# Performance work log

Hardware: AMD Instinct MI355X
Metric: run time of the kernel (lower is better)

Reference implementation:

```python
import jax, jax.numpy as jnp
import numpy as np

N_DRUG, N_MICROBE = 1500, 1572
N = N_DRUG + N_MICROBE          # 3072 nodes
F_IN = 1546                     # raw feature dim (fc1: 1546 -> 256)
D0 = 256                        # GCN input dim after fc1
H1 = H2 = 128                   # GCN hidden dims (H1 + H2 = 256)
B = 16384                       # number of (left,right) query pairs


def _sym_norm(A):
    # D^{-1/2} A D^{-1/2} (no self loops), zeros kept for isolated nodes
    deg = A.sum(axis=1)
    d = jnp.where(deg > 0, jax.lax.rsqrt(deg), 0.0)
    return A * d[:, None] * d[None, :]


def _compute_inf(adj, L):
    # dl.compute_inf: L-hop influence = L-th power of sym-normalized adjacency
    An = _sym_norm(adj)
    M = An
    for _ in range(L - 1):
        M = M @ An
    return M


def _gcn_norm(W):
    # GCNConv normalization: add self loops (weight 1), sym-normalize by weighted degree
    Ahat = W + jnp.eye(W.shape[0], dtype=W.dtype)
    deg = Ahat.sum(axis=1)
    d = jnp.where(deg > 0, jax.lax.rsqrt(deg), 0.0)
    return Ahat * d[:, None] * d[None, :]


def _glorot(key, shape):
    return jax.random.normal(key, shape, dtype=jnp.float32) / np.sqrt(shape[0])


def setup_inputs() -> dict:
    key = jax.random.key(0)
    ks = jax.random.split(key, 24)
    u = jax.random.uniform(ks[0], (N, N), dtype=jnp.float32)
    w = jax.random.uniform(ks[1], (N, N), dtype=jnp.float32)
    adj = jnp.where(u < 0.01, w, 0.0)
    adj = jnp.maximum(adj, adj.T)
    X = jax.random.normal(ks[2], (N, F_IN), dtype=jnp.float32)
    left = jax.random.randint(ks[3], (B,), 0, N)
    right = jax.random.randint(ks[4], (B,), 0, N)
    return dict(
        left=left, right=right, X=X, adj=adj, threshold=jnp.float32(1e-4),
        W_fc1=_glorot(ks[5], (F_IN, D0)), b_fc1=jnp.zeros((D0,), jnp.float32),
        Wg1=_glorot(ks[6], (D0, H1)), bg1=jnp.zeros((H1,), jnp.float32),
        Wg2=_glorot(ks[7], (H1, H2)), bg2=jnp.zeros((H2,), jnp.float32),
        Wg3=_glorot(ks[8], (D0, H1)), bg3=jnp.zeros((H1,), jnp.float32),
        Wg4=_glorot(ks[9], (H1, H2)), bg4=jnp.zeros((H2,), jnp.float32),
        Wg5=_glorot(ks[10], (D0, H1)), bg5=jnp.zeros((H1,), jnp.float32),
        Wg6=_glorot(ks[11], (H1, H2)), bg6=jnp.zeros((H2,), jnp.float32),
        cnn_k=jax.random.normal(ks[12], (1, 3, 3, 3), dtype=jnp.float32) * 0.1,
        cnn_b=jnp.zeros((1,), jnp.float32),
        W_a=_glorot(ks[13], (2 * (H1 + H2), 64)), b_a=jnp.zeros((64,), jnp.float32),
        W_b=_glorot(ks[14], (64, 2)), b_b=jnp.zeros((2,), jnp.float32),
    )


def reference(left, right, X, adj, threshold,
              W_fc1, b_fc1, Wg1, bg1, Wg2, bg2, Wg3, bg3, Wg4, bg4,
              Wg5, bg5, Wg6, bg6, cnn_k, cnn_b, W_a, b_a, W_b, b_b):
    X0 = jax.nn.relu(X @ W_fc1 + b_fc1)  # fc1: [N, 1546] -> [N, 256]

    def branch(mask_src, Wa, ba, Wb, bb):
        # dynamically thresholded edges carry the ORIGINAL adj weights
        Wadj = jnp.where(mask_src > threshold, adj, 0.0)
        An = _gcn_norm(Wadj)                       # [N, N]
        e1 = jax.nn.relu(An @ (X0 @ Wa) + ba)      # GCNConv 1
        e2 = jax.nn.relu(An @ (e1 @ Wb) + bb)      # GCNConv 2
        return jnp.concatenate([e1, e2], axis=1)   # [N, 256]

    emb_l2 = branch(_compute_inf(adj, 2), Wg1, bg1, Wg2, bg2)
    emb_l1 = branch(_compute_inf(adj, 1), Wg3, bg3, Wg4, bg4)
    emb_l0 = branch(adj, Wg5, bg5, Wg6, bg6)

    emb = jnp.stack([emb_l0, emb_l1, emb_l2], axis=0)[None]  # [1, 3, N, 256]
    conv = jax.lax.conv_general_dilated(
        emb, cnn_k, window_strides=(1, 1), padding=[(2, 2), (2, 2)],
        rhs_dilation=(2, 2), dimension_numbers=('NCHW', 'OIHW', 'NCHW'))
    emb_all = conv[0, 0] + cnn_b[0]                # [N, 256]

    pair = jnp.concatenate([emb_all[left], emb_all[right]], axis=1)  # [B, 512]
    h = jax.nn.relu(pair @ W_a + b_a)              # dropout is identity at eval
    logits = h @ W_b + b_b                         # [B, 2]
    return logits, emb_all
```

## Files before the change

### kernel.cpp

```cpp
#include <hip/hip_runtime.h>

#define NN 3072
#define FIN 1546
#define MAXR 192
#define KSPLIT 7
#define KSL 221

__global__ __launch_bounds__(256) void csr_k(const float* __restrict__ adj,
                                             int* __restrict__ cols, float* __restrict__ vals,
                                             int* __restrict__ cnt, float* __restrict__ dvec) {
    int i = blockIdx.x * 4 + (threadIdx.x >> 6);
    int lane = threadIdx.x & 63;
    const float* row = adj + (size_t)i * NN;
    float s = 0.f; int count = 0;
    int base = i * MAXR;
    for (int c = 0; c < NN; c += 64) {
        float a = row[c + lane];
        s += a;
        unsigned long long m = __ballot(a != 0.f);
        if (a != 0.f) {
            int pos = count + __popcll(m & ((1ull << lane) - 1ull));
            if (pos < MAXR) { cols[base + pos] = c + lane; vals[base + pos] = a; }
        }
        count += __popcll(m);
    }
    for (int off = 32; off; off >>= 1) s += __shfl_xor(s, off);
    if (lane == 0) {
        cnt[i] = count < MAXR ? count : MAXR;
        dvec[i] = (s > 0.f) ? 1.0f / sqrtf(s) : 0.f;
    }
}

__global__ __launch_bounds__(256) void fc1s_k(const float* __restrict__ A,
                                              const float* __restrict__ B,
                                              float* __restrict__ Cpart) {
    __shared__ float Ast[16][68];
    __shared__ float Bs[16][64];
    int tid = threadIdx.x;
    int tx = tid & 15, ty = tid >> 4;
    int i0 = blockIdx.x * 64, c0 = blockIdx.y * 64;
    int z = blockIdx.z;
    int ks = z * KSL;
    int ke = (ks + KSL < FIN) ? ks + KSL : FIN;
    int sr = tid >> 4, sk = tid & 15;
    int bk = tid >> 4, bc4 = (tid & 15) << 2;

    float ap[4]; float4 bp;
    #pragma unroll
    for (int u = 0; u < 4; u++)
        ap[u] = (ks + sk < ke) ? A[(size_t)(i0 + sr + u * 16) * FIN + ks + sk] : 0.f;
    bp = (ks + bk < ke) ? *(const float4*)&B[(size_t)(ks + bk) * 256 + c0 + bc4]
                        : make_float4(0.f, 0.f, 0.f, 0.f);

    float acc[4][4];
    #pragma unroll
    for (int r = 0; r < 4; r++)
        #pragma unroll
        for (int c = 0; c < 4; c++) acc[r][c] = 0.f;

    for (int kt = ks; kt < ke; kt += 16) {
        __syncthreads();
        #pragma unroll
        for (int u = 0; u < 4; u++) Ast[sk][sr + u * 16] = ap[u];
        *(float4*)&Bs[bk][bc4] = bp;
        __syncthreads();
        int kn = kt + 16;
        if (kn < ke) {
            #pragma unroll
            for (int u = 0; u < 4; u++)
                ap[u] = (kn + sk < ke) ? A[(size_t)(i0 + sr + u * 16) * FIN + kn + sk] : 0.f;
            bp = (kn + bk < ke) ? *(const float4*)&B[(size_t)(kn + bk) * 256 + c0 + bc4]
                                : make_float4(0.f, 0.f, 0.f, 0.f);
        }
        #pragma unroll
        for (int kk = 0; kk < 16; kk++) {
            float4 a = *(const float4*)&Ast[kk][ty * 4];
            float4 b = *(const float4*)&Bs[kk][tx * 4];
            const float* av = (const float*)&a;
            const float* bv = (const float*)&b;
            #pragma unroll
            for (int r = 0; r < 4; r++)
                #pragma unroll
                for (int c = 0; c < 4; c++) acc[r][c] += av[r] * bv[c];
        }
    }
    float* outp = Cpart + (size_t)z * NN * 256;
    #pragma unroll
    for (int r = 0; r < 4; r++) {
        int row = i0 + ty * 4 + r;
        float4 v = make_float4(acc[r][0], acc[r][1], acc[r][2], acc[r][3]);
        *(float4*)&outp[(size_t)row * 256 + c0 + tx * 4] = v;
    }
}

__global__ void reduce7_k(const float* __restrict__ Cpart, const float* __restrict__ bias,
                          float* __restrict__ X0) {
    int idx4 = blockIdx.x * 256 + threadIdx.x;
    int c4 = (idx4 & 63) << 2;
    float4 s = ((const float4*)Cpart)[idx4];
    #pragma unroll
    for (int z = 1; z < KSPLIT; z++) {
        float4 t = ((const float4*)(Cpart + (size_t)z * NN * 256))[idx4];
        s.x += t.x; s.y += t.y; s.z += t.z; s.w += t.w;
    }
    float4 b = *(const float4*)&bias[c4];
    s.x = fmaxf(s.x + b.x, 0.f); s.y = fmaxf(s.y + b.y, 0.f);
    s.z = fmaxf(s.z + b.z, 0.f); s.w = fmaxf(s.w + b.w, 0.f);
    ((float4*)X0)[idx4] = s;
}

__global__ __launch_bounds__(256) void maskall_k(const int* __restrict__ cols,
                                                 const float* __restrict__ vals,
                                                 const int* __restrict__ cnt,
                                                 const float* __restrict__ dvec,
                                                 const float* __restrict__ thrp,
                                                 int* __restrict__ mcols,
                                                 float* __restrict__ mvals,
                                                 int* __restrict__ mcnt,
                                                 float* __restrict__ db) {
    __shared__ float ds[NN];
    __shared__ int lcols[MAXR];
    __shared__ float lvals[MAXR];
    __shared__ int lcnt;
    __shared__ float osum;
    int i = blockIdx.x, tid = threadIdx.x, mode = blockIdx.y;
    mcols += (size_t)mode * NN * MAXR;
    mvals += (size_t)mode * NN * MAXR;
    mcnt  += (size_t)mode * NN;
    db    += (size_t)mode * NN;
    int ni = cnt[i], base = i * MAXR;
    float thr = *thrp;
    float di = dvec[i];

    if (mode < 2) {
        if (tid == 0) lcnt = 0;
        __syncthreads();
        float s = 0.f;
        if (tid < ni) {
            int j = cols[base + tid];
            float a = vals[base + tid];
            float m = (mode == 0) ? a : a * di * dvec[j];
            if (m > thr) {
                int p = atomicAdd(&lcnt, 1);
                mcols[base + p] = j;
                mvals[base + p] = a;
                s = a;
            }
        }
        ds[tid] = s; __syncthreads();
        for (int off = 128; off; off >>= 1) {
            if (tid < off) ds[tid] += ds[tid + off];
            __syncthreads();
        }
        if (tid == 0) {
            mcnt[i] = lcnt;
            db[i] = 1.0f / sqrtf(ds[0] + 1.0f);
        }
        return;
    }

    if (tid == 0) { osum = 0.f; lcnt = 0; }
    for (int j = tid; j < NN; j += 256) ds[j] = 0.f;
    __syncthreads();
    for (int t = tid; t < ni; t += 256) {
        int j = cols[base + t];
        float a = vals[base + t];
        lcols[t] = j; lvals[t] = a;
        ds[j] = a * dvec[j] * dvec[j];
    }
    __syncthreads();
    int lane = tid & 63, wv = tid >> 6;
    for (int o = wv; o < ni; o += 4) {
        int j = lcols[o];
        int nj = cnt[j], bj = j * MAXR;
        float dot = 0.f;
        for (int t = lane; t < nj; t += 64)
            dot += vals[bj + t] * ds[cols[bj + t]];
        for (int off = 32; off; off >>= 1) dot += __shfl_xor(dot, off);
        if (lane == 0 && di * dvec[j] * dot > thr) {
            int p = atomicAdd(&lcnt, 1);
            mcols[base + p] = j;
            mvals[base + p] = lvals[o];
            atomicAdd(&osum, lvals[o]);
        }
    }
    __syncthreads();
    if (tid == 0) {
        mcnt[i] = lcnt;
        db[i] = 1.0f / sqrtf(osum + 1.0f);
    }
}

__global__ __launch_bounds__(256) void gemm3_k(const float* __restrict__ A, int aplane, int lda,
                                               const float* __restrict__ B0,
                                               const float* __restrict__ B1,
                                               const float* __restrict__ B2,
                                               int K, float* __restrict__ out) {
    __shared__ float Ast[16][68];
    __shared__ float Bs[16][64];
    int tid = threadIdx.x;
    int tx = tid & 15, ty = tid >> 4;
    int i0 = blockIdx.x * 64, c0 = blockIdx.y * 64;
    int z = blockIdx.z;
    const float* Ab = A + (size_t)z * aplane;
    const float* B = (z == 0) ? B0 : (z == 1) ? B1 : B2;
    float* outp = out + (size_t)z * NN * 128;
    int sr = tid >> 4, sk = tid & 15;
    int bk = tid >> 4, bc4 = (tid & 15) << 2;

    float ap[4]; float4 bp;
    #pragma unroll
    for (int u = 0; u < 4; u++) ap[u] = Ab[(size_t)(i0 + sr + u * 16) * lda + sk];
    bp = *(const float4*)&B[(size_t)bk * 128 + c0 + bc4];

    float acc[4][4];
    #pragma unroll
    for (int r = 0; r < 4; r++)
        #pragma unroll
        for (int c = 0; c < 4; c++) acc[r][c] = 0.f;

    for (int kt = 0; kt < K; kt += 16) {
        __syncthreads();
        #pragma unroll
        for (int u = 0; u < 4; u++) Ast[sk][sr + u * 16] = ap[u];
        *(float4*)&Bs[bk][bc4] = bp;
        __syncthreads();
        int kn = kt + 16;
        if (kn < K) {
            #pragma unroll
            for (int u = 0; u < 4; u++) ap[u] = Ab[(size_t)(i0 + sr + u * 16) * lda + kn + sk];
            bp = *(const float4*)&B[(size_t)(kn + bk) * 128 + c0 + bc4];
        }
        #pragma unroll
        for (int kk = 0; kk < 16; kk++) {
            float4 a = *(const float4*)&Ast[kk][ty * 4];
            float4 b = *(const float4*)&Bs[kk][tx * 4];
            const float* av = (const float*)&a;
            const float* bv = (const float*)&b;
            #pragma unroll
            for (int r = 0; r < 4; r++)
                #pragma unroll
                for (int c = 0; c < 4; c++) acc[r][c] += av[r] * bv[c];
        }
    }
    #pragma unroll
    for (int r = 0; r < 4; r++) {
        int row = i0 + ty * 4 + r;
        float4 v = make_float4(acc[r][0], acc[r][1], acc[r][2], acc[r][3]);
        *(float4*)&outp[(size_t)row * 128 + c0 + tx * 4] = v;
    }
}

__global__ __launch_bounds__(256) void spmm3_k(const int* __restrict__ mcols,
                                               const float* __restrict__ mvals,
                                               const int* __restrict__ mcnt,
                                               const float* __restrict__ db,
                                               const float* __restrict__ Xin,
                                               const float* __restrict__ bias0,
                                               const float* __restrict__ bias1,
                                               const float* __restrict__ bias2,
                                               float* __restrict__ outA,
                                               float* __restrict__ embf, int coff) {
    __shared__ float lcoef[MAXR];
    __shared__ int lj[MAXR];
    __shared__ float4 part[8][32];
    int i = blockIdx.x, tid = threadIdx.x, b = blockIdx.y;
    mcols += (size_t)b * NN * MAXR;
    mvals += (size_t)b * NN * MAXR;
    mcnt  += (size_t)b * NN;
    db    += (size_t)b * NN;
    const float* Xb = Xin + (size_t)b * NN * 128;
    const float* bias = (b == 0) ? bias0 : (b == 1) ? bias1 : bias2;
    float dbi = db[i];
    int n = mcnt[i], base = i * MAXR;
    if (tid < n) {
        int j = mcols[base + tid];
        lj[tid] = j;
        lcoef[tid] = mvals[base + tid] * dbi * db[j];
    }
    __syncthreads();
    int g = tid >> 5, c4 = (tid & 31) << 2;
    float4 acc = make_float4(0.f, 0.f, 0.f, 0.f);
    if (g == 0) {
        float4 x = *(const float4*)&Xb[(size_t)i * 128 + c4];
        float d2 = dbi * dbi;
        acc = make_float4(d2 * x.x, d2 * x.y, d2 * x.z, d2 * x.w);
    }
    for (int t = g; t < n; t += 8) {
        float cf = lcoef[t];
        float4 x = *(const float4*)&Xb[(size_t)lj[t] * 128 + c4];
        acc.x += cf * x.x; acc.y += cf * x.y; acc.z += cf * x.z; acc.w += cf * x.w;
    }
    part[g][tid & 31] = acc;
    __syncthreads();
    if (tid < 32) {
        float4 s = part[0][tid];
        #pragma unroll
        for (int gg = 1; gg < 8; gg++) {
            float4 t4 = part[gg][tid];
            s.x += t4.x; s.y += t4.y; s.z += t4.z; s.w += t4.w;
        }
        int cc = tid << 2;
        float4 bv = *(const float4*)&bias[cc];
        s.x = fmaxf(s.x + bv.x, 0.f); s.y = fmaxf(s.y + bv.y, 0.f);
        s.z = fmaxf(s.z + bv.z, 0.f); s.w = fmaxf(s.w + bv.w, 0.f);
        if (outA) *(float4*)&outA[((size_t)b * NN + i) * 128 + cc] = s;
        *(float4*)&embf[((size_t)b * NN + i) * 256 + coff + cc] = s;
    }
}

__global__ __launch_bounds__(256) void conv3f_k(const float* __restrict__ emb,
                                                const float* __restrict__ ck,
                                                const float* __restrict__ cb,
                                                float* __restrict__ outf) {
    __shared__ float rows[3][3][256];
    int n = blockIdx.x, c = threadIdx.x;
    #pragma unroll
    for (int i = 0; i < 3; i++)
        #pragma unroll
        for (int kh = 0; kh < 3; kh++) {
            int nn2 = n + 2 * kh - 2;
            rows[i][kh][c] = (nn2 >= 0 && nn2 < NN) ? emb[((size_t)i * NN + nn2) * 256 + c] : 0.f;
        }
    __syncthreads();
    float s = cb[0];
    #pragma unroll
    for (int i = 0; i < 3; i++)
        #pragma unroll
        for (int kh = 0; kh < 3; kh++)
            #pragma unroll
            for (int kw = 0; kw < 3; kw++) {
                int cc = c + 2 * kw - 2;
                if (cc >= 0 && cc < 256)
                    s += rows[i][kh][cc] * ck[(i * 3 + kh) * 3 + kw];
            }
    outf[(size_t)n * 256 + c] = s;
}

__global__ __launch_bounds__(256) void gemmUV_k(const float* __restrict__ A,
                                                const float* __restrict__ Wa,
                                                float* __restrict__ uvp) {
    __shared__ float Ast[16][68];
    __shared__ float Bs[16][64];
    int tid = threadIdx.x;
    int tx = tid & 15, ty = tid >> 4;
    int i0 = blockIdx.x * 64;
    int half = blockIdx.y;
    int z = blockIdx.z;
    int ks = z * 128;
    const float* Bb = Wa + (half ? 256 * 64 : 0);
    int sr = tid >> 4, sk = tid & 15;
    int bk = tid >> 4, bc4 = (tid & 15) << 2;

    float ap[4]; float4 bp;
    #pragma unroll
    for (int u = 0; u < 4; u++) ap[u] = A[(size_t)(i0 + sr + u * 16) * 256 + ks + sk];
    bp = *(const float4*)&Bb[(size_t)(ks + bk) * 64 + bc4];

    float acc[4][4];
    #pragma unroll
    for (int r = 0; r < 4; r++)
        #pragma unroll
        for (int c = 0; c < 4; c++) acc[r][c] = 0.f;

    for (int kt = ks; kt < ks + 128; kt += 16) {
        __syncthreads();
        #pragma unroll
        for (int u = 0; u < 4; u++) Ast[sk][sr + u * 16] = ap[u];
        *(float4*)&Bs[bk][bc4] = bp;
        __syncthreads();
        int kn = kt + 16;
        if (kn < ks + 128) {
            #pragma unroll
            for (int u = 0; u < 4; u++) ap[u] = A[(size_t)(i0 + sr + u * 16) * 256 + kn + sk];
            bp = *(const float4*)&Bb[(size_t)(kn + bk) * 64 + bc4];
        }
        #pragma unroll
        for (int kk = 0; kk < 16; kk++) {
            float4 a = *(const float4*)&Ast[kk][ty * 4];
            float4 b = *(const float4*)&Bs[kk][tx * 4];
            const float* av = (const float*)&a;
            const float* bv = (const float*)&b;
            #pragma unroll
            for (int r = 0; r < 4; r++)
                #pragma unroll
                for (int c = 0; c < 4; c++) acc[r][c] += av[r] * bv[c];
        }
    }
    float* outp = uvp + (size_t)z * NN * 128;
    #pragma unroll
    for (int r = 0; r < 4; r++) {
        int row = i0 + ty * 4 + r;
        float4 v = make_float4(acc[r][0], acc[r][1], acc[r][2], acc[r][3]);
        *(float4*)&outp[(size_t)row * 128 + half * 64 + tx * 4] = v;
    }
}

__global__ __launch_bounds__(256) void pairuv_k(const int* __restrict__ left,
                                                const int* __restrict__ right,
                                                const float* __restrict__ uvp,
                                                const float* __restrict__ ba,
                                                const float* __restrict__ Wb,
                                                const float* __restrict__ bb,
                                                float* __restrict__ out) {
    int tid = threadIdx.x;
    int w = tid >> 6, c = tid & 63;
    int base = blockIdx.x * 16 + w * 4;
    const float* u0 = uvp;
    const float* u1 = uvp + (size_t)NN * 128;
    float bac = ba[c];
    float w0 = Wb[c * 2], w1 = Wb[c * 2 + 1];
    float b0 = bb[0], b1 = bb[1];
    #pragma unroll
    for (int pp = 0; pp < 4; pp++) {
        int row = base + pp;
        int l = left[row], r = right[row];
        float h = u0[(size_t)l * 128 + c] + u1[(size_t)l * 128 + c]
                + u0[(size_t)r * 128 + 64 + c] + u1[(size_t)r * 128 + 64 + c] + bac;
        h = fmaxf(h, 0.f);
        float s0 = h * w0, s1 = h * w1;
        for (int off = 32; off; off >>= 1) {
            s0 += __shfl_xor(s0, off);
            s1 += __shfl_xor(s1, off);
        }
        if (c == 0) {
            out[row * 2]     = s0 + b0;
            out[row * 2 + 1] = s1 + b1;
        }
    }
}

extern "C" void kernel_launch(void* const* d_in, const int* in_sizes, int n_in,
                              void* d_out, int out_size, void* d_ws, size_t ws_size,
                              hipStream_t stream) {
    const int* left  = (const int*)d_in[0];
    const int* right = (const int*)d_in[1];
    const float* X    = (const float*)d_in[2];
    const float* adj  = (const float*)d_in[3];
    const float* thr  = (const float*)d_in[4];
    const float* Wfc1 = (const float*)d_in[5];
    const float* bfc1 = (const float*)d_in[6];
    const float* Wga[3] = { (const float*)d_in[15], (const float*)d_in[11], (const float*)d_in[7] };
    const float* bga[3] = { (const float*)d_in[16], (const float*)d_in[12], (const float*)d_in[8] };
    const float* Wgb[3] = { (const float*)d_in[17], (const float*)d_in[13], (const float*)d_in[9] };
    const float* bgb[3] = { (const float*)d_in[18], (const float*)d_in[14], (const float*)d_in[10] };
    const float* cnnk = (const float*)d_in[19];
    const float* cnnb = (const float*)d_in[20];
    const float* Wa_  = (const float*)d_in[21];
    const float* ba_  = (const float*)d_in[22];
    const float* Wb_  = (const float*)d_in[23];
    const float* bb_  = (const float*)d_in[24];

    char* p = (char*)d_ws;
    auto take = [&](size_t n) { char* q = p; p += (n + 255) & ~(size_t)255; return q; };
    float* dvec = (float*)take(NN * 4);
    float* db3  = (float*)take((size_t)3 * NN * 4);
    int*   cnt  = (int*)take(NN * 4);
    int*   mcnt3 = (int*)take((size_t)3 * NN * 4);
    int*   cols = (int*)take((size_t)NN * MAXR * 4);
    float* vals = (float*)take((size_t)NN * MAXR * 4);
    int*   mcols3 = (int*)take((size_t)3 * NN * MAXR * 4);
    float* mvals3 = (float*)take((size_t)3 * NN * MAXR * 4);
    float* X0    = (float*)take((size_t)NN * 256 * 4);
    float* XWall = (float*)take((size_t)3 * NN * 128 * 4);
    float* e1all = (float*)take((size_t)3 * NN * 128 * 4);
    float* HW2all= (float*)take((size_t)3 * NN * 128 * 4);
    float* embf  = (float*)take((size_t)3 * NN * 256 * 4);
    float* Cpart = XWall;
    float* uvp = embf;

    float* out_logits = (float*)d_out;
    float* out_emb = out_logits + 32768;

    csr_k<<<NN / 4, 256, 0, stream>>>(adj, cols, vals, cnt, dvec);
    fc1s_k<<<dim3(NN / 64, 4, KSPLIT), 256, 0, stream>>>(X, Wfc1, Cpart);
    reduce7_k<<<NN * 64 / 256, 256, 0, stream>>>(Cpart, bfc1, X0);

    maskall_k<<<dim3(NN, 3), 256, 0, stream>>>(cols, vals, cnt, dvec, thr,
                                               mcols3, mvals3, mcnt3, db3);

    gemm3_k<<<dim3(NN / 64, 2, 3), 256, 0, stream>>>(X0, 0, 256, Wga[0], Wga[1], Wga[2], 256, XWall);
    spmm3_k<<<dim3(NN, 3), 256, 0, stream>>>(mcols3, mvals3, mcnt3, db3, XWall,
                                             bga[0], bga[1], bga[2], e1all, embf, 0);
    gemm3_k<<<dim3(NN / 64, 2, 3), 256, 0, stream>>>(e1all, NN * 128, 128, Wgb[0], Wgb[1], Wgb[2], 128, HW2all);
    spmm3_k<<<dim3(NN, 3), 256, 0, stream>>>(mcols3, mvals3, mcnt3, db3, HW2all,
                                             bgb[0], bgb[1], bgb[2], (float*)0, embf, 128);

    conv3f_k<<<NN, 256, 0, stream>>>(embf, cnnk, cnnb, out_emb);
    gemmUV_k<<<dim3(NN / 64, 2, 2), 256, 0, stream>>>(out_emb, Wa_, uvp);
    pairuv_k<<<16384 / 16, 256, 0, stream>>>(left, right, uvp, ba_, Wb_, bb_, out_logits);
}
```

Baseline: 339.2 us.

## Compute fc1 with bf16x3 split MFMA instead of FP32 SIMT GEMM

```diff
diff --git a/kernel.cpp b/kernel.cpp
--- a/kernel.cpp
+++ b/kernel.cpp
@@ -2,9 +2,13 @@
 
 #define NN 3072
 #define FIN 1546
+#define KP 1568
 #define MAXR 192
 #define KSPLIT 7
-#define KSL 221
+#define KSLICE 224
+
+typedef __attribute__((ext_vector_type(8))) __bf16 bf16x8;
+typedef __attribute__((ext_vector_type(4))) float f32x4;
 
 __global__ __launch_bounds__(256) void csr_k(const float* __restrict__ adj,
                                              int* __restrict__ cols, float* __restrict__ vals,
@@ -31,65 +35,69 @@
     }
 }
 
-__global__ __launch_bounds__(256) void fc1s_k(const float* __restrict__ A,
-                                              const float* __restrict__ B,
+__global__ void xsplit_k(const float* __restrict__ X, __bf16* __restrict__ Xh,
+                         __bf16* __restrict__ Xl) {
+    int idx = blockIdx.x * 256 + threadIdx.x;
+    int i = idx / KP, c = idx - i * KP;
+    float x = (c < FIN) ? X[(size_t)i * FIN + c] : 0.f;
+    __bf16 h = (__bf16)x;
+    Xh[idx] = h;
+    Xl[idx] = (__bf16)(x - (float)h);
+}
+
+__global__ void wsplit_k(const float* __restrict__ W, __bf16* __restrict__ WhT,
+                         __bf16* __restrict__ WlT) {
+    int idx = blockIdx.x * 256 + threadIdx.x;
+    int c = idx / KP, k = idx - c * KP;
+    float x = (k < FIN) ? W[(size_t)k * 256 + c] : 0.f;
+    __bf16 h = (__bf16)x;
+    WhT[idx] = h;
+    WlT[idx] = (__bf16)(x - (float)h);
+}
+
+__global__ __launch_bounds__(256) void fc1m_k(const __bf16* __restrict__ Xh,
+                                              const __bf16* __restrict__ Xl,
+                                              const __bf16* __restrict__ WhT,
+                                              const __bf16* __restrict__ WlT,
                                               float* __restrict__ Cpart) {
-    __shared__ float Ast[16][68];
-    __shared__ float Bs[16][64];
     int tid = threadIdx.x;
-    int tx = tid & 15, ty = tid >> 4;
+    int w = tid >> 6, lane = tid & 63;
+    int m = lane & 15, q = lane >> 4;
     int i0 = blockIdx.x * 64, c0 = blockIdx.y * 64;
     int z = blockIdx.z;
-    int ks = z * KSL;
-    int ke = (ks + KSL < FIN) ? ks + KSL : FIN;
-    int sr = tid >> 4, sk = tid & 15;
-    int bk = tid >> 4, bc4 = (tid & 15) << 2;
-
-    float ap[4]; float4 bp;
-    #pragma unroll
-    for (int u = 0; u < 4; u++)
-        ap[u] = (ks + sk < ke) ? A[(size_t)(i0 + sr + u * 16) * FIN + ks + sk] : 0.f;
-    bp = (ks + bk < ke) ? *(const float4*)&B[(size_t)(ks + bk) * 256 + c0 + bc4]
-                        : make_float4(0.f, 0.f, 0.f, 0.f);
-
-    float acc[4][4];
-    #pragma unroll
-    for (int r = 0; r < 4; r++)
-        #pragma unroll
-        for (int c = 0; c < 4; c++) acc[r][c] = 0.f;
-
-    for (int kt = ks; kt < ke; kt += 16) {
-        __syncthreads();
-        #pragma unroll
-        for (int u = 0; u < 4; u++) Ast[sk][sr + u * 16] = ap[u];
-        *(float4*)&Bs[bk][bc4] = bp;
-        __syncthreads();
-        int kn = kt + 16;
-        if (kn < ke) {
-            #pragma unroll
-            for (int u = 0; u < 4; u++)
-                ap[u] = (kn + sk < ke) ? A[(size_t)(i0 + sr + u * 16) * FIN + kn + sk] : 0.f;
-            bp = (kn + bk < ke) ? *(const float4*)&B[(size_t)(kn + bk) * 256 + c0 + bc4]
-                                : make_float4(0.f, 0.f, 0.f, 0.f);
-        }
-        #pragma unroll
-        for (int kk = 0; kk < 16; kk++) {
-            float4 a = *(const float4*)&Ast[kk][ty * 4];
-            float4 b = *(const float4*)&Bs[kk][tx * 4];
-            const float* av = (const float*)&a;
-            const float* bv = (const float*)&b;
-            #pragma unroll
-            for (int r = 0; r < 4; r++)
-                #pragma unroll
-                for (int c = 0; c < 4; c++) acc[r][c] += av[r] * bv[c];
+    int k0 = z * KSLICE;
+    int rowA = i0 + w * 16 + m;
+    const __bf16* xh = Xh + (size_t)rowA * KP + k0 + q * 8;
+    const __bf16* xl = Xl + (size_t)rowA * KP + k0 + q * 8;
+    const __bf16* bh0 = WhT + (size_t)(c0 + m) * KP + k0 + q * 8;
+    const __bf16* bl0 = WlT + (size_t)(c0 + m) * KP + k0 + q * 8;
+
+    f32x4 acc[4];
+    #pragma unroll
+    for (int ct = 0; ct < 4; ct++)
+        #pragma unroll
+        for (int r = 0; r < 4; r++) acc[ct][r] = 0.f;
+
+    for (int ks = 0; ks < KSLICE; ks += 32) {
+        bf16x8 ah = *(const bf16x8*)(xh + ks);
+        bf16x8 al = *(const bf16x8*)(xl + ks);
+        #pragma unroll
+        for (int ct = 0; ct < 4; ct++) {
+            bf16x8 bh = *(const bf16x8*)(bh0 + (size_t)ct * 16 * KP + ks);
+            bf16x8 bl = *(const bf16x8*)(bl0 + (size_t)ct * 16 * KP + ks);
+            acc[ct] = __builtin_amdgcn_mfma_f32_16x16x32_bf16(ah, bh, acc[ct], 0, 0, 0);
+            acc[ct] = __builtin_amdgcn_mfma_f32_16x16x32_bf16(ah, bl, acc[ct], 0, 0, 0);
+            acc[ct] = __builtin_amdgcn_mfma_f32_16x16x32_bf16(al, bh, acc[ct], 0, 0, 0);
         }
     }
     float* outp = Cpart + (size_t)z * NN * 256;
-    #pragma unroll
-    for (int r = 0; r < 4; r++) {
-        int row = i0 + ty * 4 + r;
-        float4 v = make_float4(acc[r][0], acc[r][1], acc[r][2], acc[r][3]);
-        *(float4*)&outp[(size_t)row * 256 + c0 + tx * 4] = v;
+    int rowBase = i0 + w * 16 + q * 4;
+    #pragma unroll
+    for (int ct = 0; ct < 4; ct++) {
+        int col = c0 + ct * 16 + m;
+        #pragma unroll
+        for (int r = 0; r < 4; r++)
+            outp[(size_t)(rowBase + r) * 256 + col] = acc[ct][r];
     }
 }
 
@@ -466,6 +474,10 @@
     float* e1all = (float*)take((size_t)3 * NN * 128 * 4);
     float* HW2all= (float*)take((size_t)3 * NN * 128 * 4);
     float* embf  = (float*)take((size_t)3 * NN * 256 * 4);
+    __bf16* Xl   = (__bf16*)take((size_t)NN * KP * 2);
+    __bf16* WhT  = (__bf16*)take((size_t)256 * KP * 2);
+    __bf16* WlT  = (__bf16*)take((size_t)256 * KP * 2);
+    __bf16* Xh = (__bf16*)mcols3;
     float* Cpart = XWall;
     float* uvp = embf;
 
@@ -473,7 +485,9 @@
     float* out_emb = out_logits + 32768;
 
     csr_k<<<NN / 4, 256, 0, stream>>>(adj, cols, vals, cnt, dvec);
-    fc1s_k<<<dim3(NN / 64, 4, KSPLIT), 256, 0, stream>>>(X, Wfc1, Cpart);
+    xsplit_k<<<NN * KP / 256, 256, 0, stream>>>(X, Xh, Xl);
+    wsplit_k<<<256 * KP / 256, 256, 0, stream>>>(Wfc1, WhT, WlT);
+    fc1m_k<<<dim3(NN / 64, 4, KSPLIT), 256, 0, stream>>>(Xh, Xl, WhT, WlT, Cpart);
     reduce7_k<<<NN * 64 / 256, 256, 0, stream>>>(Cpart, bfc1, X0);
 
     maskall_k<<<dim3(NN, 3), 256, 0, stream>>>(cols, vals, cnt, dvec, thr,
```

New measurement: 335.1 us. No clear change (-1.2%).
